# Kernel tuning notes

Measured on AMD Instinct MI355X. Metric: run time of the kernel, lower is better.

Reference implementation:

```python
import jax, jax.numpy as jnp
import numpy as np

N_HEADS = 8
D_MODEL = 128
EPS = 1e-6


def setup_inputs() -> dict:
    key = jax.random.key(0)
    k1, k2, k3, k4, k5 = jax.random.split(key, 5)
    B, Dim, F, T = 1, D_MODEL, 256, 1024
    queries = jax.random.normal(k1, (B, Dim, F, T), dtype=jnp.float32)
    keys = jax.random.normal(k2, (B, Dim, F, T), dtype=jnp.float32)
    values = jax.random.normal(k3, (B, Dim, F, T), dtype=jnp.float32)
    # out_projection: Linear(d_model, d_output) with d_output == d_model
    W_out = jax.random.normal(k4, (D_MODEL, D_MODEL), dtype=jnp.float32) / np.sqrt(D_MODEL)
    b_out = jax.random.normal(k5, (D_MODEL,), dtype=jnp.float32) * 0.01
    return {"queries": queries, "keys": keys, "values": values,
            "W_out": W_out, "b_out": b_out}


def _to_heads(x, B, Dim, L, H):
    # (B, Dim, F, T) -> (B, L, Dim) -> (B, L, H, d) -> (B, H, L, d)
    return x.reshape(B, Dim, L).transpose(0, 2, 1).reshape(B, L, H, Dim // H).transpose(0, 2, 1, 3)


def reference(queries, keys, values, W_out, b_out):
    B, Dim, F, T = queries.shape
    L = F * T
    H = N_HEADS
    q = jax.nn.sigmoid(_to_heads(queries, B, Dim, L, H))  # (B,H,L,d)
    k = jax.nn.sigmoid(_to_heads(keys, B, Dim, L, H))
    v = _to_heads(values, B, Dim, L, H)

    # NOTE: sums are over the HEAD axis (dim=1), faithful to the original code
    ks = k.sum(axis=1, keepdims=True)                      # (B,1,L,d)
    qs = q.sum(axis=1, keepdims=True)
    sink_incoming = 1.0 / jnp.sum((q + EPS) * (ks + EPS), axis=-1)      # (B,H,L)
    source_outgoing = 1.0 / jnp.sum((k + EPS) * (qs + EPS), axis=-1)    # (B,H,L)
    conserved_sink = jnp.sum(
        (q + EPS) * ((k * source_outgoing[..., None]).sum(axis=1, keepdims=True) + EPS),
        axis=-1)                                                        # (B,H,L)
    conserved_source = jnp.sum(
        (k + EPS) * ((q * sink_incoming[..., None]).sum(axis=1, keepdims=True) + EPS),
        axis=-1)
    conserved_source = jnp.clip(conserved_source, -1.0, 1.0)
    sink_allocation = jax.nn.sigmoid(conserved_sink * (float(L) / float(L)))
    source_competition = jax.nn.softmax(conserved_source, axis=-1) * float(L)

    kv = jnp.einsum('bhld,bhlm->bhdm', k, v * source_competition[..., None])
    qkv = jnp.einsum('bhld,bhdm->bhlm', q * sink_incoming[..., None], kv)
    x = (qkv * sink_allocation[..., None]).transpose(0, 2, 1, 3).reshape(B, L, Dim)
    x = x @ W_out.T + b_out                                 # dropout is identity (eval)
    return x.transpose(0, 2, 1).reshape(B, Dim, F, T)
```

## Files before the change

kernel.cpp:

```cpp
#include <hip/hip_runtime.h>
#include <hip/hip_bf16.h>

#define L_TOT (1 << 18)
#define L_SHIFT 18
#define NHEAD 8
#define DHEAD 16
#define DMODEL 128
#define EPSF 1e-6f

typedef float f32x4 __attribute__((ext_vector_type(4)));
typedef short bf16x8 __attribute__((ext_vector_type(8)));

__device__ __forceinline__ float frcp(float x) { return __builtin_amdgcn_rcpf(x); }
__device__ __forceinline__ float sigm(float x) { return frcp(1.0f + __expf(-x)); }
__device__ __forceinline__ unsigned short f2bf(float f) {
    return (unsigned short)((__float_as_uint(f) + 0x8000u) >> 16);
}

__device__ __forceinline__ float qsum(float x) {
    x += __int_as_float(__builtin_amdgcn_update_dpp(0, __float_as_int(x), 0xB1, 0xf, 0xf, true));
    x += __int_as_float(__builtin_amdgcn_update_dpp(0, __float_as_int(x), 0x4E, 0xf, 0xf, true));
    return x;
}

__global__ __launch_bounds__(256) void k1_stats(
        const float* __restrict__ Q, const float* __restrict__ K,
        float* __restrict__ scale_o, float* __restrict__ wbuf,
        float* __restrict__ sep) {
    __shared__ unsigned int sp[64][128];
    __shared__ float wlds[8][64];
    __shared__ float slds[8][64];

    const int t = threadIdx.x;
    const int l0 = blockIdx.x * 64;

    {
        const int cS = t & 63;
        const int w = t >> 6;
        const int swS = (cS & 31) << 2;
#pragma unroll
        for (int i = 0; i < 8; ++i) {
            const int pb = 4 * (w + 4 * i);
            unsigned pk[4];
#pragma unroll
            for (int r = 0; r < 4; ++r) {
                float qv = sigm(Q[((pb + r) << L_SHIFT) + l0 + cS]);
                float kv = sigm(K[((pb + r) << L_SHIFT) + l0 + cS]);
                unsigned qu = __float_as_uint(qv) + 0x8000u;
                unsigned ku = __float_as_uint(kv) + 0x8000u;
                pk[r] = (ku & 0xffff0000u) | (qu >> 16);
            }
            *(uint4*)(&sp[cS][pb ^ swS]) = make_uint4(pk[0], pk[1], pk[2], pk[3]);
        }
    }
    __syncthreads();

    const int c = t >> 2;
    const int s = t & 3;
    const int sw = (c & 31) << 2;

    unsigned a[32];
#pragma unroll
    for (int h = 0; h < 8; ++h) {
        const uint4 v = *(const uint4*)&sp[c][(h * 16 + s * 4) ^ sw];
        a[h * 4 + 0] = v.x; a[h * 4 + 1] = v.y;
        a[h * 4 + 2] = v.z; a[h * 4 + 3] = v.w;
    }

    float ks[4] = {0.f, 0.f, 0.f, 0.f}, qs[4] = {0.f, 0.f, 0.f, 0.f};
#pragma unroll
    for (int h = 0; h < 8; ++h)
#pragma unroll
        for (int j = 0; j < 4; ++j) {
            const unsigned u = a[h * 4 + j];
            qs[j] += __uint_as_float(u << 16);
            ks[j] += __uint_as_float(u & 0xffff0000u);
        }

    float kse[4], qse[4];
#pragma unroll
    for (int j = 0; j < 4; ++j) { kse[j] = ks[j] + EPSF; qse[j] = qs[j] + EPSF; }

    float si[8], so[8];
#pragma unroll
    for (int h = 0; h < 8; ++h) {
        float aq = 0.f, ak = 0.f;
#pragma unroll
        for (int j = 0; j < 4; ++j) {
            const unsigned u = a[h * 4 + j];
            aq += (__uint_as_float(u << 16) + EPSF) * kse[j];
            ak += (__uint_as_float(u & 0xffff0000u) + EPSF) * qse[j];
        }
        si[h] = frcp(qsum(aq));
        so[h] = frcp(qsum(ak));
    }

    float kso[4] = {0.f, 0.f, 0.f, 0.f}, qsi[4] = {0.f, 0.f, 0.f, 0.f};
#pragma unroll
    for (int h = 0; h < 8; ++h)
#pragma unroll
        for (int j = 0; j < 4; ++j) {
            const unsigned u = a[h * 4 + j];
            kso[j] += __uint_as_float(u & 0xffff0000u) * so[h];
            qsi[j] += __uint_as_float(u << 16) * si[h];
        }
#pragma unroll
    for (int j = 0; j < 4; ++j) { kse[j] = kso[j] + EPSF; qse[j] = qsi[j] + EPSF; }

    float e2[2], sc2[2];
#pragma unroll
    for (int h = 0; h < 8; ++h) {
        float aq = 0.f, ak = 0.f;
#pragma unroll
        for (int j = 0; j < 4; ++j) {
            const unsigned u = a[h * 4 + j];
            aq += (__uint_as_float(u << 16) + EPSF) * kse[j];
            ak += (__uint_as_float(u & 0xffff0000u) + EPSF) * qse[j];
        }
        const float ck = qsum(aq);
        float cs = qsum(ak);
        if ((h >> 1) == s) {
            cs = fminf(fmaxf(cs, -1.f), 1.f);
            e2[h & 1] = __expf(cs);
            sc2[h & 1] = sigm(ck) * si[h];
        }
    }
    wlds[2 * s + 0][c] = e2[0];
    wlds[2 * s + 1][c] = e2[1];
    slds[2 * s + 0][c] = sc2[0];
    slds[2 * s + 1][c] = sc2[1];
    __syncthreads();

    {
        float v = wlds[t >> 5][t & 31] + wlds[t >> 5][32 + (t & 31)];
        v += __shfl_xor(v, 16, 64);
        v += __shfl_xor(v, 8, 64);
        v += __shfl_xor(v, 4, 64);
        v += __shfl_xor(v, 2, 64);
        v += __shfl_xor(v, 1, 64);
        if ((t & 31) == 0) sep[blockIdx.x * 8 + (t >> 5)] = v;
    }

#pragma unroll
    for (int i = 0; i < 2; ++i) {
        const int idx = t + i * 256;
        const int h = idx >> 6, cc = idx & 63;
        wbuf[(h << L_SHIFT) + l0 + cc] = wlds[h][cc];
        scale_o[(h << L_SHIFT) + l0 + cc] = slds[h][cc];
    }
}

__global__ __launch_bounds__(256) void k2_kv(
        const float* __restrict__ Kg, const float* __restrict__ Vg,
        const float* __restrict__ wg, float* __restrict__ parts) {
    const int b = blockIdx.x;
    const int h = b >> 6;
    const int blk = b & 63;
    const int t = threadIdx.x;
    const int dd = t >> 4, m = t & 15;

    __shared__ float A[16][132];
    __shared__ float Vv[16][132];
    __shared__ float wl[128];

    const int baseK = (h * DHEAD) << L_SHIFT;
    float acc = 0.f;

    for (int ch = 0; ch < 32; ++ch) {
        const int l0 = blk * 4096 + ch * 128;
        __syncthreads();
        if (t < 128) wl[t] = wg[(h << L_SHIFT) + l0 + t];
        __syncthreads();
#pragma unroll
        for (int i = 0; i < 2; ++i) {
            const int e = t + i * 256;
            const int r = e >> 5, c4 = e & 31;
            const float4 kq = *(const float4*)&Kg[baseK + (r << L_SHIFT) + l0 + c4 * 4];
            const float4 vq = *(const float4*)&Vg[baseK + (r << L_SHIFT) + l0 + c4 * 4];
            A[r][c4 * 4 + 0] = sigm(kq.x) * wl[c4 * 4 + 0];
            A[r][c4 * 4 + 1] = sigm(kq.y) * wl[c4 * 4 + 1];
            A[r][c4 * 4 + 2] = sigm(kq.z) * wl[c4 * 4 + 2];
            A[r][c4 * 4 + 3] = sigm(kq.w) * wl[c4 * 4 + 3];
            *(float4*)&Vv[r][c4 * 4] = vq;
        }
        __syncthreads();
#pragma unroll
        for (int c4 = 0; c4 < 32; ++c4) {
            const float4 av = *(const float4*)&A[dd][c4 * 4];
            const float4 vv = *(const float4*)&Vv[m][c4 * 4];
            acc += av.x * vv.x + av.y * vv.y + av.z * vv.z + av.w * vv.w;
        }
    }
    parts[b * 256 + t] = acc;
}

__global__ __launch_bounds__(256) void k3_wkv(
        const float* __restrict__ Wg, const float* __restrict__ parts,
        const float* __restrict__ sep, unsigned* __restrict__ wkvb) {
    const int hb = blockIdx.x;
    const int t = threadIdx.x;
    __shared__ float kvf[256];
    __shared__ float redl[4];

    float p = 0.f;
#pragma unroll
    for (int i = 0; i < 16; ++i) p += sep[(t + i * 256) * 8 + hb];
#pragma unroll
    for (int o = 32; o >= 1; o >>= 1) p += __shfl_xor(p, o, 64);
    if ((t & 63) == 0) redl[t >> 6] = p;

    float kacc = 0.f;
    for (int j = 0; j < 64; ++j)
        kacc += parts[(hb * 64 + j) * 256 + t];

    __syncthreads();
    const float s = (float)L_TOT / (redl[0] + redl[1] + redl[2] + redl[3]);
    kvf[t] = kacc * s;
    __syncthreads();

#pragma unroll
    for (int i = 0; i < 4; ++i) {
        const int j = t + i * 256;
        const int dim = j & 127, prp = j >> 7;
        float a0 = 0.f, a1 = 0.f;
#pragma unroll
        for (int mm = 0; mm < 16; ++mm) {
            const float wv = Wg[dim * 128 + hb * 16 + mm];
            a0 += wv * kvf[(2 * prp) * 16 + mm];
            a1 += wv * kvf[(2 * prp + 1) * 16 + mm];
        }
        wkvb[dim * 64 + hb * 8 + prp] = ((unsigned)f2bf(a1) << 16) | f2bf(a0);
    }
}

__global__ __launch_bounds__(256) void k4_mfma(
        const float* __restrict__ Q, const float* __restrict__ scale_g,
        const unsigned* __restrict__ wkvb, const float* __restrict__ bg,
        float* __restrict__ out) {
    __shared__ unsigned A_lds[128 * 68];
    __shared__ float bias[128];
    const int t = threadIdx.x;

#pragma unroll
    for (int i = 0; i < 8; ++i) {
        const int idx4 = t + i * 256;
        const uint4 v = ((const uint4*)wkvb)[idx4];
        const int row = idx4 >> 4, c4 = idx4 & 15;
        *(uint4*)&A_lds[row * 68 + c4 * 4] = v;
    }
    if (t < 128) bias[t] = bg[t];
    __syncthreads();

    const int w = t >> 6, lane = t & 63;
    const int lq = lane & 15, lh = lane >> 4;

#pragma unroll
    for (int ci = 0; ci < 2; ++ci) {
        const int l = blockIdx.x * 128 + ci * 64 + w * 16 + lq;

        float qv[4][8];
        float scv[4];
#pragma unroll
        for (int ks = 0; ks < 4; ++ks) {
            scv[ks] = scale_g[((ks * 2 + (lane >> 5)) << L_SHIFT) + l];
#pragma unroll
            for (int j = 0; j < 8; ++j) {
                const int p = ks * 32 + lh * 8 + j;
                qv[ks][j] = Q[(p << L_SHIFT) + l];
            }
        }
        bf16x8 bfr[4];
#pragma unroll
        for (int ks = 0; ks < 4; ++ks)
#pragma unroll
            for (int j = 0; j < 8; ++j)
                bfr[ks][j] = (short)f2bf(sigm(qv[ks][j]) * scv[ks]);

        f32x4 acc[8];
#pragma unroll
        for (int mt = 0; mt < 8; ++mt)
            acc[mt] = *(const f32x4*)&bias[mt * 16 + lh * 4];

#pragma unroll
        for (int ks = 0; ks < 4; ++ks) {
#pragma unroll
            for (int mt = 0; mt < 8; ++mt) {
                const int row = mt * 16 + lq;
                const bf16x8 aA = *(const bf16x8*)&A_lds[row * 68 + ks * 16 + lh * 4];
                acc[mt] = __builtin_amdgcn_mfma_f32_16x16x32_bf16(aA, bfr[ks], acc[mt], 0, 0, 0);
            }
        }

#pragma unroll
        for (int mt = 0; mt < 8; ++mt) {
#pragma unroll
            for (int r = 0; r < 4; ++r) {
                const int dim = mt * 16 + lh * 4 + r;
                out[(dim << L_SHIFT) + l] = acc[mt][r];
            }
        }
    }
}

extern "C" void kernel_launch(void* const* d_in, const int* in_sizes, int n_in,
                              void* d_out, int out_size, void* d_ws, size_t ws_size,
                              hipStream_t stream) {
    const float* Q = (const float*)d_in[0];
    const float* K = (const float*)d_in[1];
    const float* V = (const float*)d_in[2];
    const float* W = (const float*)d_in[3];
    const float* B = (const float*)d_in[4];
    float* out = (float*)d_out;
    float* ws = (float*)d_ws;

    float* parts    = ws;
    unsigned* wkvb  = (unsigned*)(ws + 131072);
    float* sep      = ws + 139264;
    float* scale    = ws + 172032;
    float* wbuf     = scale + 8 * L_TOT;

    k1_stats<<<L_TOT / 64, 256, 0, stream>>>(Q, K, scale, wbuf, sep);
    k2_kv<<<NHEAD * 64, 256, 0, stream>>>(K, V, wbuf, parts);
    k3_wkv<<<NHEAD, 256, 0, stream>>>(W, parts, sep, wkvb);
    k4_mfma<<<L_TOT / 128, 256, 0, stream>>>(Q, scale, wkvb, B, out);
}
```

Before: 220.1 us.

## Load Q/K directly per thread in stats kernel, drop LDS transpose staging

The stats kernel no longer stages sigmoid'd Q/K through a 32KB shared-memory transpose buffer. Each thread now loads its own 32 channel values directly from global memory. Per-position outputs are written straight to global, and the per-head exp sums are reduced with shuffles plus a small shared array. This removes LDS traffic and a barrier and raises occupancy by shrinking shared memory. In exchange, the global loads are less coalesced: each group of 4 threads shares a column, so each wavefront reads only 16 contiguous floats per channel row, and the stores to wbuf and scale_o are similarly strided.

```diff
diff --git a/kernel.cpp b/kernel.cpp
--- a/kernel.cpp
+++ b/kernel.cpp
@@ -27,44 +27,30 @@
         const float* __restrict__ Q, const float* __restrict__ K,
         float* __restrict__ scale_o, float* __restrict__ wbuf,
         float* __restrict__ sep) {
-    __shared__ unsigned int sp[64][128];
-    __shared__ float wlds[8][64];
-    __shared__ float slds[8][64];
+    __shared__ float hredl[4][8];
 
     const int t = threadIdx.x;
     const int l0 = blockIdx.x * 64;
-
-    {
-        const int cS = t & 63;
-        const int w = t >> 6;
-        const int swS = (cS & 31) << 2;
-#pragma unroll
-        for (int i = 0; i < 8; ++i) {
-            const int pb = 4 * (w + 4 * i);
-            unsigned pk[4];
-#pragma unroll
-            for (int r = 0; r < 4; ++r) {
-                float qv = sigm(Q[((pb + r) << L_SHIFT) + l0 + cS]);
-                float kv = sigm(K[((pb + r) << L_SHIFT) + l0 + cS]);
-                unsigned qu = __float_as_uint(qv) + 0x8000u;
-                unsigned ku = __float_as_uint(kv) + 0x8000u;
-                pk[r] = (ku & 0xffff0000u) | (qu >> 16);
-            }
-            *(uint4*)(&sp[cS][pb ^ swS]) = make_uint4(pk[0], pk[1], pk[2], pk[3]);
-        }
-    }
-    __syncthreads();
-
     const int c = t >> 2;
     const int s = t & 3;
-    const int sw = (c & 31) << 2;
+    const int l = l0 + c;
+
+    float qv[32], kv[32];
+#pragma unroll
+    for (int h = 0; h < 8; ++h)
+#pragma unroll
+        for (int r = 0; r < 4; ++r) {
+            const int p = h * 16 + s * 4 + r;
+            qv[h * 4 + r] = Q[(p << L_SHIFT) + l];
+            kv[h * 4 + r] = K[(p << L_SHIFT) + l];
+        }
 
     unsigned a[32];
 #pragma unroll
-    for (int h = 0; h < 8; ++h) {
-        const uint4 v = *(const uint4*)&sp[c][(h * 16 + s * 4) ^ sw];
-        a[h * 4 + 0] = v.x; a[h * 4 + 1] = v.y;
-        a[h * 4 + 2] = v.z; a[h * 4 + 3] = v.w;
+    for (int i = 0; i < 32; ++i) {
+        const unsigned qu = __float_as_uint(sigm(qv[i])) + 0x8000u;
+        const unsigned ku = __float_as_uint(sigm(kv[i])) + 0x8000u;
+        a[i] = (ku & 0xffff0000u) | (qu >> 16);
     }
 
     float ks[4] = {0.f, 0.f, 0.f, 0.f}, qs[4] = {0.f, 0.f, 0.f, 0.f};
@@ -125,29 +111,25 @@
             sc2[h & 1] = sigm(ck) * si[h];
         }
     }
-    wlds[2 * s + 0][c] = e2[0];
-    wlds[2 * s + 1][c] = e2[1];
-    slds[2 * s + 0][c] = sc2[0];
-    slds[2 * s + 1][c] = sc2[1];
+
+    wbuf[((2 * s + 0) << L_SHIFT) + l] = e2[0];
+    wbuf[((2 * s + 1) << L_SHIFT) + l] = e2[1];
+    scale_o[((2 * s + 0) << L_SHIFT) + l] = sc2[0];
+    scale_o[((2 * s + 1) << L_SHIFT) + l] = sc2[1];
+
+    float v0 = e2[0], v1 = e2[1];
+    v0 += __shfl_xor(v0, 4, 64);  v1 += __shfl_xor(v1, 4, 64);
+    v0 += __shfl_xor(v0, 8, 64);  v1 += __shfl_xor(v1, 8, 64);
+    v0 += __shfl_xor(v0, 16, 64); v1 += __shfl_xor(v1, 16, 64);
+    v0 += __shfl_xor(v0, 32, 64); v1 += __shfl_xor(v1, 32, 64);
+    if ((t & 63) < 4) {
+        const int w = t >> 6;
+        hredl[w][2 * s + 0] = v0;
+        hredl[w][2 * s + 1] = v1;
+    }
     __syncthreads();
-
-    {
-        float v = wlds[t >> 5][t & 31] + wlds[t >> 5][32 + (t & 31)];
-        v += __shfl_xor(v, 16, 64);
-        v += __shfl_xor(v, 8, 64);
-        v += __shfl_xor(v, 4, 64);
-        v += __shfl_xor(v, 2, 64);
-        v += __shfl_xor(v, 1, 64);
-        if ((t & 31) == 0) sep[blockIdx.x * 8 + (t >> 5)] = v;
-    }
-
-#pragma unroll
-    for (int i = 0; i < 2; ++i) {
-        const int idx = t + i * 256;
-        const int h = idx >> 6, cc = idx & 63;
-        wbuf[(h << L_SHIFT) + l0 + cc] = wlds[h][cc];
-        scale_o[(h << L_SHIFT) + l0 + cc] = slds[h][cc];
-    }
+    if (t < 8)
+        sep[blockIdx.x * 8 + t] = hredl[0][t] + hredl[1][t] + hredl[2][t] + hredl[3][t];
 }
 
 __global__ __launch_bounds__(256) void k2_kv(
```

After: 222.1 us. No clear change (+0.9%).
